# Kernel optimization log

Hardware: AMD Instinct MI355X
Metric: run time of the kernel (lower is better)

The kernel has to match this reference:

```python
import jax, jax.numpy as jnp
import numpy as np

PATCH = 16
IMG = 457
PAD = 7
HEADS = 8
NEG = -1e30        # finite stand-in for -inf (underflows to exactly 0 after softmax)


def layernorm(x, w, b):
    m = jnp.mean(x, axis=-1, keepdims=True)
    v = jnp.var(x, axis=-1, keepdims=True)
    return (x - m) / jnp.sqrt(v + 1e-5) * w + b


def shifted_patch_tokenize(x, w, b):
    # x: [B, C, H, W] (H, W multiples of PATCH)
    p = PATCH
    B, C, H, W = x.shape
    h = p // 2
    # torch order: (dx, dy) pairs, rolled as shifts=(dy, dx) over dims (2, 3)
    shifts = [(0, 0), (-h, -h), (h, -h), (-h, h), (h, h)]
    xs = jnp.concatenate(
        [jnp.roll(x, shift=(dy, dx), axis=(2, 3)) for dx, dy in shifts], axis=1
    )  # [B, 5C, H, W]
    Hp, Wp = H // p, W // p
    t = xs.reshape(B, 5 * C, Hp, p, Wp, p)
    t = t.transpose(0, 2, 4, 1, 3, 5).reshape(B, Hp * Wp, 5 * C * p * p)
    return t @ w.T + b  # [B, N, dim]


def locality_self_attention(x, scale, wqkv, wout, bout):
    # x: [B, N, C]; scale: [heads, 1, 1]
    B, N, C = x.shape
    dh = C // HEADS
    qkv = x @ wqkv.T  # [B, N, 3C]
    q, k, v = jnp.split(qkv, 3, axis=-1)
    q, k, v = [t.reshape(B, N, HEADS, dh).transpose(0, 2, 1, 3) for t in (q, k, v)]
    dots = jnp.einsum('bhid,bhjd->bhij', q, k) * scale[None]  # [B, H, N, N]
    idx = jnp.arange(N)
    mask = idx[None, :] >= idx[:, None]  # strict upper triangle + diagonal masked
    dots = jnp.where(mask, NEG, dots)
    attn = jax.nn.softmax(dots, axis=-1)
    # row 0 is fully masked (torch produces NaN here; we define it as 0 attention)
    attn = jnp.where(idx[:, None] == 0, 0.0, attn)
    out = jnp.einsum('bhij,bhjd->bhid', attn, v)
    out = out.transpose(0, 2, 1, 3).reshape(B, N, C)
    return out @ wout.T + bout


def reference(x, pos_emb, spt_w, spt_b, ln1_w, ln1_b, scale, wqkv, wout, bout,
              ln2_w, ln2_b, ff1_w, ff1_b, ff2_w, ff2_b, pix_w, pix_b):
    xp = jnp.pad(x, ((0, 0), (0, 0), (0, PAD), (0, PAD)))
    B, C, H, W = xp.shape
    p = PATCH
    Hp, Wp = H // p, W // p
    t = shifted_patch_tokenize(xp, spt_w, spt_b) + pos_emb  # [B, N, dim]
    depth = ln1_w.shape[0]
    for d in range(depth):
        t = locality_self_attention(layernorm(t, ln1_w[d], ln1_b[d]),
                                    scale[d], wqkv[d], wout[d], bout[d]) + t
        h = layernorm(t, ln2_w[d], ln2_b[d])
        h = jax.nn.gelu(h @ ff1_w[d].T + ff1_b[d], approximate=False)
        t = h @ ff2_w[d].T + ff2_b[d] + t
    pix = t @ pix_w.T + pix_b  # [B, N, C*p*p]
    out = pix.reshape(B, Hp, Wp, C, p, p).transpose(0, 3, 1, 4, 2, 5).reshape(B, C, H, W)
    return out[:, :, :IMG, :IMG]


def setup_inputs():
    key = jax.random.key(0)
    ks = jax.random.split(key, 10)
    B, Cin, dim, depth = 8, 1, 256, 3
    Np = 29 * 29  # padded 464/16 = 29 patches per side

    def rn(k, shape, sc=0.02):
        return jax.random.normal(k, shape, dtype=jnp.float32) * sc

    return {
        'x': jax.random.normal(ks[0], (B, Cin, IMG, IMG), dtype=jnp.float32),
        'pos_emb': rn(ks[1], (1, Np, dim), 1.0),
        'spt_w': rn(ks[2], (dim, Cin * 5 * PATCH * PATCH)),
        'spt_b': jnp.zeros((dim,), jnp.float32),
        'ln1_w': jnp.ones((depth, dim), jnp.float32),
        'ln1_b': jnp.zeros((depth, dim), jnp.float32),
        'scale': jnp.ones((depth, HEADS, 1, 1), jnp.float32),
        'wqkv': rn(ks[3], (depth, 3 * dim, dim)),
        'wout': rn(ks[4], (depth, dim, dim)),
        'bout': jnp.zeros((depth, dim), jnp.float32),
        'ln2_w': jnp.ones((depth, dim), jnp.float32),
        'ln2_b': jnp.zeros((depth, dim), jnp.float32),
        'ff1_w': rn(ks[5], (depth, 4 * dim, dim)),
        'ff1_b': jnp.zeros((depth, 4 * dim), jnp.float32),
        'ff2_w': rn(ks[6], (depth, dim, 4 * dim)),
        'ff2_b': jnp.zeros((depth, dim), jnp.float32),
        'pix_w': rn(ks[7], (Cin * PATCH * PATCH, dim)),
        'pix_b': jnp.zeros((Cin * PATCH * PATCH,), jnp.float32),
    }
```

## Files before the change

kernel.cpp:

```cpp
#include <hip/hip_runtime.h>
#include <hip/hip_bf16.h>
#include <math.h>

typedef __hip_bfloat16 bf16;
typedef short bf16x8 __attribute__((ext_vector_type(8)));
typedef float floatx4 __attribute__((ext_vector_type(4)));

#define NTOK 841
#define BATCH 8
#define DIM 256
#define HEADS 8
#define DH 32
#define IMG 457
#define HPAD 464
#define ROWS (BATCH * NTOK)
#define LDA 40

#define W_SPT   0
#define W_QKV   327680
#define W_OUT   917504
#define W_FF1   1114112
#define W_FF2   1900544
#define W_PIX   2686976
#define W_TOTAL 2752512

__device__ __forceinline__ float fast_gelu(float v) {
    float x = v * 0.70710678118654752f;
    float ax = fabsf(x);
    float t = __builtin_amdgcn_rcpf(1.0f + 0.3275911f * ax);
    float p = t * (0.254829592f +
              t * (-0.284496736f +
              t * (1.421413741f +
              t * (-1.453152027f +
              t * 1.061405429f))));
    float e = __expf(-x * x);
    float erfa = 1.0f - p * e;
    float erfx = copysignf(erfa, x);
    return 0.5f * v * (1.0f + erfx);
}

__global__ __launch_bounds__(256) void wconv_kernel(
    const float* __restrict__ s_spt, const float* __restrict__ s_qkv,
    const float* __restrict__ s_out, const float* __restrict__ s_ff1,
    const float* __restrict__ s_ff2, const float* __restrict__ s_pix,
    bf16* __restrict__ dst) {
    int idx = (blockIdx.x * 256 + threadIdx.x) * 4;
    const float* src; int off;
    if      (idx < W_QKV) { src = s_spt; off = W_SPT; }
    else if (idx < W_OUT) { src = s_qkv; off = W_QKV; }
    else if (idx < W_FF1) { src = s_out; off = W_OUT; }
    else if (idx < W_FF2) { src = s_ff1; off = W_FF1; }
    else if (idx < W_PIX) { src = s_ff2; off = W_FF2; }
    else                  { src = s_pix; off = W_PIX; }
    float4 v = *(const float4*)(src + (idx - off));
    union { ushort4 u; bf16 h[4]; } pk;
    pk.h[0] = __float2bfloat16(v.x);
    pk.h[1] = __float2bfloat16(v.y);
    pk.h[2] = __float2bfloat16(v.z);
    pk.h[3] = __float2bfloat16(v.w);
    *(ushort4*)(dst + idx) = pk.u;
}

__global__ __launch_bounds__(256) void tokenize_kernel(const float* __restrict__ x,
                                                       bf16* __restrict__ tok) {
    int idx = blockIdx.x * 256 + threadIdx.x;
    int gm = idx / 320;
    int k4 = (idx - gm * 320) * 4;
    int b = gm / NTOK;
    int n = gm - b * NTOK;
    int hp = n / 29, wp = n - (n / 29) * 29;
    int c = k4 >> 8;
    int py = (k4 >> 4) & 15;
    int px0 = k4 & 15;
    const int dxs[5] = {0, -8, 8, -8, 8};
    const int dys[5] = {0, -8, -8, 8, 8};
    int r = hp * 16 + py - dys[c];
    r += (r < 0) ? HPAD : 0; r -= (r >= HPAD) ? HPAD : 0;
    bool rok = (r < IMG);
    union { ushort4 u; bf16 h[4]; } pk;
#pragma unroll
    for (int i = 0; i < 4; i++) {
        int s = wp * 16 + px0 + i - dxs[c];
        s += (s < 0) ? HPAD : 0; s -= (s >= HPAD) ? HPAD : 0;
        float v = 0.0f;
        if (rok && s < IMG) v = x[((size_t)b * IMG + r) * IMG + s];
        pk.h[i] = __float2bfloat16(v);
    }
    *(ushort4*)(tok + (size_t)gm * 1280 + k4) = pk.u;
}

template <int BM, int BN>
__global__ __launch_bounds__(256) void gemm_db_kernel(
    const bf16* __restrict__ A, const bf16* __restrict__ W,
    const float* __restrict__ bias, const float* __restrict__ resid,
    const float* __restrict__ posemb, float* __restrict__ Cf,
    bf16* __restrict__ Cb, int M, int N, int K, int act) {
    constexpr int WM = BM / 2, WN = BN / 2;
    constexpr int TI = WM / 16, TJ = WN / 16;
    constexpr int ACHUNKS = BM * 4;
    constexpr int BCHUNKS = BN * 4;
    static_assert(ACHUNKS <= 256 && BCHUNKS <= 256, "one chunk per thread");
    __shared__ bf16 As[2][BM * LDA];
    __shared__ bf16 Bs[2][BN * LDA];
    const int tid = threadIdx.x;
    const int m0 = blockIdx.y * BM, n0 = blockIdx.x * BN;
    const int w = tid >> 6, lane = tid & 63;
    const int wm = (w >> 1) * WM, wn = (w & 1) * WN;
    const int li = lane & 15, quad = lane >> 4;

    floatx4 acc[TI][TJ] = {};
    float4 a0, b0, a1, b1;

    const int arow = tid >> 2, ako = (tid & 3) << 3;
    const bool a_on = tid < ACHUNKS;
    const bool b_on = tid < BCHUNKS;

    auto load_a = [&](float4& ar, int k0) {
        if (a_on) {
            int gm = m0 + arow;
            ar = make_float4(0.f, 0.f, 0.f, 0.f);
            if (gm < M) ar = *(const float4*)(A + (size_t)gm * K + k0 + ako);
        }
    };
    auto load_b = [&](float4& br, int k0) {
        if (b_on) br = *(const float4*)(W + (size_t)(n0 + arow) * K + k0 + ako);
    };
    auto store_ab = [&](int buf, const float4& ar, const float4& br) {
        if (a_on) *(float4*)&As[buf][arow * LDA + ako] = ar;
        if (b_on) *(float4*)&Bs[buf][arow * LDA + ako] = br;
    };
    auto compute = [&](int buf) {
        bf16x8 af[TI], bfr[TJ];
#pragma unroll
        for (int t = 0; t < TI; t++)
            af[t] = *(const bf16x8*)&As[buf][(wm + t * 16 + li) * LDA + quad * 8];
#pragma unroll
        for (int t = 0; t < TJ; t++)
            bfr[t] = *(const bf16x8*)&Bs[buf][(wn + t * 16 + li) * LDA + quad * 8];
#pragma unroll
        for (int ti = 0; ti < TI; ti++)
#pragma unroll
            for (int tj = 0; tj < TJ; tj++)
                acc[ti][tj] = __builtin_amdgcn_mfma_f32_16x16x32_bf16(
                    af[ti], bfr[tj], acc[ti][tj], 0, 0, 0);
    };

    const int ktiles = K >> 5;
    load_a(a0, 0); load_b(b0, 0);
    store_ab(0, a0, b0);
    if (ktiles > 1) { load_a(a0, 32); load_b(b0, 32); }
    if (ktiles > 2) { load_a(a1, 64); load_b(b1, 64); }
    __syncthreads();

    for (int kt = 0; kt < ktiles; kt += 2) {
        compute(0);
        if (kt + 1 < ktiles) store_ab(1, a0, b0);
        if (kt + 3 < ktiles) { load_a(a0, (kt + 3) << 5); load_b(b0, (kt + 3) << 5); }
        __syncthreads();
        compute(1);
        if (kt + 2 < ktiles) store_ab(0, a1, b1);
        if (kt + 4 < ktiles) { load_a(a1, (kt + 4) << 5); load_b(b1, (kt + 4) << 5); }
        __syncthreads();
    }

#pragma unroll
    for (int ti = 0; ti < TI; ti++) {
#pragma unroll
        for (int r = 0; r < 4; r++) {
            int gm = m0 + wm + ti * 16 + quad * 4 + r;
            if (gm >= M) continue;
#pragma unroll
            for (int tj = 0; tj < TJ; tj++) {
                int gn = n0 + wn + tj * 16 + li;
                float v = acc[ti][tj][r];
                if (bias) v += bias[gn];
                if (act == 1) v = fast_gelu(v);
                if (posemb) v += posemb[(size_t)(gm % NTOK) * N + gn];
                if (resid) v += resid[(size_t)gm * N + gn];
                if (Cf) Cf[(size_t)gm * N + gn] = v;
                if (Cb) Cb[(size_t)gm * N + gn] = __float2bfloat16(v);
            }
        }
    }
}

__global__ __launch_bounds__(256) void ln_kernel(const float* __restrict__ in,
                                                 const float* __restrict__ w,
                                                 const float* __restrict__ b,
                                                 bf16* __restrict__ out) {
    const int lane = threadIdx.x & 63;
    const int wv = threadIdx.x >> 6;
    const size_t row = (size_t)blockIdx.x * 4 + wv;
    const int c = lane * 4;
    float4 x = *(const float4*)&in[row * DIM + c];
    float s = x.x + x.y + x.z + x.w;
    float s2 = x.x * x.x + x.y * x.y + x.z * x.z + x.w * x.w;
#pragma unroll
    for (int off = 1; off < 64; off <<= 1) {
        s += __shfl_xor(s, off);
        s2 += __shfl_xor(s2, off);
    }
    float mean = s * (1.0f / DIM);
    float var = s2 * (1.0f / DIM) - mean * mean;
    float rstd = rsqrtf(var + 1e-5f);
    float4 w4 = *(const float4*)&w[c];
    float4 b4 = *(const float4*)&b[c];
    union { ushort4 u; bf16 h[4]; } pk;
    pk.h[0] = __float2bfloat16((x.x - mean) * rstd * w4.x + b4.x);
    pk.h[1] = __float2bfloat16((x.y - mean) * rstd * w4.y + b4.y);
    pk.h[2] = __float2bfloat16((x.z - mean) * rstd * w4.z + b4.z);
    pk.h[3] = __float2bfloat16((x.w - mean) * rstd * w4.w + b4.w);
    *(ushort4*)&out[row * DIM + c] = pk.u;
}

#define LQ 40
#define LP 72
__global__ __launch_bounds__(256) void attn_mfma_kernel(
    const bf16* __restrict__ qkv, const float* __restrict__ scale,
    bf16* __restrict__ out) {
    __shared__ bf16 Qs[64 * LQ];
    __shared__ bf16 Ks[2][64 * LQ];
    __shared__ bf16 Vt[2][32 * LP];
    __shared__ bf16 Ps[64 * LP];

    const int tid = threadIdx.x;
    const int bh = blockIdx.x;
    const int b = bh >> 3, h = bh & 7;
    const int it = (int)gridDim.y - 1 - (int)blockIdx.y;
    const int i0 = it * 64;
    const float sc = scale[h];
    const float sc2 = sc * 1.44269504f;
    const float mshift = -8.0f * 1.44269504f;
    const bf16* base = qkv + (size_t)b * NTOK * 768 + h * DH;

    const int w = tid >> 6, lane = tid & 63;
    const int li = lane & 15, quad = lane >> 4;
    const int srow = tid >> 2, sd0 = (tid & 3) * 8;
    const int vcol = (srow + ((tid & 3) << 4)) & 63;

    {
        int gi = i0 + srow;
        bf16x8 v = {};
        if (gi < NTOK) v = *(const bf16x8*)(base + (size_t)gi * 768 + sd0);
        *(bf16x8*)&Qs[srow * LQ + sd0] = v;
    }
    bf16x8 kreg = {}, vreg = {};
    {
        int gj = srow;
        if (gj < NTOK) {
            kreg = *(const bf16x8*)(base + (size_t)gj * 768 + 256 + sd0);
            vreg = *(const bf16x8*)(base + (size_t)gj * 768 + 512 + sd0);
        }
    }
    __syncthreads();
    const bf16x8 aq = *(const bf16x8*)&Qs[(w * 16 + li) * LQ + quad * 8];

    const bf16x8 ones8 = {(short)0x3F80, (short)0x3F80, (short)0x3F80, (short)0x3F80,
                          (short)0x3F80, (short)0x3F80, (short)0x3F80, (short)0x3F80};

    floatx4 o[2] = {};
    floatx4 o2 = {};
    const bool interior_ok = (i0 + 63 < NTOK);

    for (int jt = 0; jt <= it; jt++) {
        const int j0 = jt * 64;
        const int cur = jt & 1;
        *(bf16x8*)&Ks[cur][srow * LQ + sd0] = kreg;
#pragma unroll
        for (int u = 0; u < 8; u++) Vt[cur][(sd0 + u) * LP + vcol] = ((bf16*)&vreg)[u];
        if (jt < it) {
            int gj = j0 + 64 + srow;
            kreg = bf16x8{};
            vreg = bf16x8{};
            if (gj < NTOK) {
                kreg = *(const bf16x8*)(base + (size_t)gj * 768 + 256 + sd0);
                vreg = *(const bf16x8*)(base + (size_t)gj * 768 + 512 + sd0);
            }
        }
        __syncthreads();

        floatx4 sacc[4];
#pragma unroll
        for (int tj = 0; tj < 4; tj++) {
            bf16x8 bk = *(const bf16x8*)&Ks[cur][(tj * 16 + li) * LQ + quad * 8];
            floatx4 z = {};
            sacc[tj] = __builtin_amdgcn_mfma_f32_16x16x32_bf16(aq, bk, z, 0, 0, 0);
        }

        if (jt < it && interior_ok) {
#pragma unroll
            for (int r = 0; r < 4; r++) {
#pragma unroll
                for (int tj = 0; tj < 4; tj++) {
                    float p = exp2f(fmaf(sacc[tj][r], sc2, mshift));
                    Ps[(w * 16 + quad * 4 + r) * LP + tj * 16 + li] = __float2bfloat16(p);
                }
            }
        } else {
#pragma unroll
            for (int r = 0; r < 4; r++) {
                const int gi = i0 + w * 16 + quad * 4 + r;
#pragma unroll
                for (int tj = 0; tj < 4; tj++) {
                    bool ok = (j0 + tj * 16 + li < gi) && (gi < NTOK);
                    float arg = ok ? fmaf(sacc[tj][r], sc2, mshift) : -1e30f;
                    float p = exp2f(arg);
                    Ps[(w * 16 + quad * 4 + r) * LP + tj * 16 + li] = __float2bfloat16(p);
                }
            }
        }

#pragma unroll
        for (int kk = 0; kk < 64; kk += 32) {
            bf16x8 ap = *(const bf16x8*)&Ps[(w * 16 + li) * LP + kk + quad * 8];
#pragma unroll
            for (int td = 0; td < 2; td++) {
                const int kr = (2 * td + (li >> 3)) & 3;
                const int vc0 = (kk + quad * 8 + (kr << 4)) & 63;
                bf16x8 bv = *(const bf16x8*)&Vt[cur][(td * 16 + li) * LP + vc0];
                o[td] = __builtin_amdgcn_mfma_f32_16x16x32_bf16(ap, bv, o[td], 0, 0, 0);
            }
            o2 = __builtin_amdgcn_mfma_f32_16x16x32_bf16(ap, ones8, o2, 0, 0, 0);
        }
    }

#pragma unroll
    for (int r = 0; r < 4; r++) {
        int gi = i0 + w * 16 + quad * 4 + r;
        if (gi >= NTOK) continue;
        float l = o2[r];
        float iv = (gi > 0 && l > 0.0f) ? 1.0f / l : 0.0f;
        bf16* op = out + ((size_t)b * NTOK + gi) * DIM + h * DH;
        op[li]      = __float2bfloat16(o[0][r] * iv);
        op[16 + li] = __float2bfloat16(o[1][r] * iv);
    }
}

__global__ __launch_bounds__(256) void scatter_kernel(const float* __restrict__ pix,
                                                      float* __restrict__ out) {
    const size_t total = (size_t)BATCH * IMG * IMG;
    size_t idx = (size_t)blockIdx.x * 256 + threadIdx.x;
    if (idx >= total) return;
    int b = (int)(idx / ((size_t)IMG * IMG));
    int rem = (int)(idx % ((size_t)IMG * IMG));
    int r = rem / IMG, col = rem % IMG;
    int hp = r >> 4, py = r & 15;
    int wp = col >> 4, px = col & 15;
    out[idx] = pix[((size_t)b * NTOK + hp * 29 + wp) * DIM + py * 16 + px];
}

extern "C" void kernel_launch(void* const* d_in, const int* in_sizes, int n_in,
                              void* d_out, int out_size, void* d_ws, size_t ws_size,
                              hipStream_t stream) {
    const float* x     = (const float*)d_in[0];
    const float* pos   = (const float*)d_in[1];
    const float* sptw  = (const float*)d_in[2];
    const float* sptb  = (const float*)d_in[3];
    const float* ln1w  = (const float*)d_in[4];
    const float* ln1b  = (const float*)d_in[5];
    const float* scale = (const float*)d_in[6];
    const float* wqkv  = (const float*)d_in[7];
    const float* wout  = (const float*)d_in[8];
    const float* bout  = (const float*)d_in[9];
    const float* ln2w  = (const float*)d_in[10];
    const float* ln2b  = (const float*)d_in[11];
    const float* ff1w  = (const float*)d_in[12];
    const float* ff1b  = (const float*)d_in[13];
    const float* ff2w  = (const float*)d_in[14];
    const float* ff2b  = (const float*)d_in[15];
    const float* pixw  = (const float*)d_in[16];
    const float* pixb  = (const float*)d_in[17];
    float* out = (float*)d_out;

    const size_t NT = (size_t)ROWS * DIM;
    char* ws = (char*)d_ws;
    float* t    = (float*)ws;                         ws += NT * 4;
    bf16*  tn_b = (bf16*)ws;                          ws += NT * 2;
    bf16*  t_b  = (bf16*)ws;                          ws += NT * 2;
    bf16*  ao_b = (bf16*)ws;                          ws += NT * 2;
    bf16*  wbf  = (bf16*)ws;                          ws += (size_t)W_TOTAL * 2;
    char*  big  = ws;
    bf16*  tok   = (bf16*)big;
    bf16*  qkv_b = (bf16*)big;
    bf16*  ffh   = (bf16*)big;
    float* pixo  = (float*)big;

    wconv_kernel<<<W_TOTAL / 4 / 256, 256, 0, stream>>>(sptw, wqkv, wout, ff1w,
                                                        ff2w, pixw, wbf);
    tokenize_kernel<<<(ROWS * 320) / 256, 256, 0, stream>>>(x, tok);
    gemm_db_kernel<32, 64><<<dim3(4, 211), 256, 0, stream>>>(
        tok, wbf + W_SPT, sptb, nullptr, pos, t, nullptr, ROWS, DIM, 1280, 0);

    for (int d = 0; d < 3; d++) {
        ln_kernel<<<ROWS / 4, 256, 0, stream>>>(t, ln1w + d * DIM, ln1b + d * DIM, tn_b);
        gemm_db_kernel<64, 64><<<dim3(12, 106), 256, 0, stream>>>(
            tn_b, wbf + W_QKV + (size_t)d * 768 * DIM, nullptr, nullptr, nullptr,
            nullptr, qkv_b, ROWS, 768, DIM, 0);
        {
            dim3 grid(BATCH * HEADS, (NTOK + 63) / 64);
            attn_mfma_kernel<<<grid, 256, 0, stream>>>(qkv_b, scale + d * HEADS, ao_b);
        }
        gemm_db_kernel<32, 64><<<dim3(4, 211), 256, 0, stream>>>(
            ao_b, wbf + W_OUT + (size_t)d * DIM * DIM, bout + d * DIM, t, nullptr,
            t, nullptr, ROWS, DIM, DIM, 0);
        ln_kernel<<<ROWS / 4, 256, 0, stream>>>(t, ln2w + d * DIM, ln2b + d * DIM, tn_b);
        gemm_db_kernel<64, 64><<<dim3(16, 106), 256, 0, stream>>>(
            tn_b, wbf + W_FF1 + (size_t)d * 1024 * DIM, ff1b + d * 1024, nullptr,
            nullptr, nullptr, ffh, ROWS, 1024, DIM, 1);
        gemm_db_kernel<32, 64><<<dim3(4, 211), 256, 0, stream>>>(
            ffh, wbf + W_FF2 + (size_t)d * DIM * 1024, ff2b + d * DIM, t, nullptr,
            t, (d == 2) ? t_b : nullptr, ROWS, DIM, 1024, 0);
    }

    gemm_db_kernel<32, 64><<<dim3(4, 211), 256, 0, stream>>>(
        t_b, wbf + W_PIX, pixb, nullptr, nullptr, pixo, nullptr, ROWS, DIM, DIM, 0);
    {
        size_t total = (size_t)BATCH * IMG * IMG;
        scatter_kernel<<<dim3((unsigned)((total + 255) / 256)), 256, 0, stream>>>(pixo, out);
    }
}
```

Measured before the change: 335.8 us.

## Split-K with atomic residual accumulation for out-proj and FF2 GEMMs

Result: slower. 559.2 us (+66.5%).

```diff
diff --git a/kernel.cpp b/kernel.cpp
--- a/kernel.cpp
+++ b/kernel.cpp
@@ -94,7 +94,7 @@
     const bf16* __restrict__ A, const bf16* __restrict__ W,
     const float* __restrict__ bias, const float* __restrict__ resid,
     const float* __restrict__ posemb, float* __restrict__ Cf,
-    bf16* __restrict__ Cb, int M, int N, int K, int act) {
+    bf16* __restrict__ Cb, int M, int N, int K, int act, int kspl, int aF32) {
     constexpr int WM = BM / 2, WN = BN / 2;
     constexpr int TI = WM / 16, TJ = WN / 16;
     constexpr int ACHUNKS = BM * 4;
@@ -119,7 +119,25 @@
         if (a_on) {
             int gm = m0 + arow;
             ar = make_float4(0.f, 0.f, 0.f, 0.f);
-            if (gm < M) ar = *(const float4*)(A + (size_t)gm * K + k0 + ako);
+            if (gm < M) {
+                if (aF32) {
+                    const float* Af = (const float*)A;
+                    float4 u0 = *(const float4*)(Af + (size_t)gm * K + k0 + ako);
+                    float4 u1 = *(const float4*)(Af + (size_t)gm * K + k0 + ako + 4);
+                    union { float4 f; ushort s[8]; } pk;
+                    pk.s[0] = __bfloat16_as_ushort(__float2bfloat16(u0.x));
+                    pk.s[1] = __bfloat16_as_ushort(__float2bfloat16(u0.y));
+                    pk.s[2] = __bfloat16_as_ushort(__float2bfloat16(u0.z));
+                    pk.s[3] = __bfloat16_as_ushort(__float2bfloat16(u0.w));
+                    pk.s[4] = __bfloat16_as_ushort(__float2bfloat16(u1.x));
+                    pk.s[5] = __bfloat16_as_ushort(__float2bfloat16(u1.y));
+                    pk.s[6] = __bfloat16_as_ushort(__float2bfloat16(u1.z));
+                    pk.s[7] = __bfloat16_as_ushort(__float2bfloat16(u1.w));
+                    ar = pk.f;
+                } else {
+                    ar = *(const float4*)(A + (size_t)gm * K + k0 + ako);
+                }
+            }
         }
     };
     auto load_b = [&](float4& br, int k0) {
@@ -145,22 +163,44 @@
                     af[ti], bfr[tj], acc[ti][tj], 0, 0, 0);
     };
 
-    const int ktiles = K >> 5;
-    load_a(a0, 0); load_b(b0, 0);
+    const int ktotal = K >> 5;
+    const int kts = ktotal / kspl;
+    const int ktb = blockIdx.z * kts;
+    load_a(a0, ktb << 5); load_b(b0, ktb << 5);
     store_ab(0, a0, b0);
-    if (ktiles > 1) { load_a(a0, 32); load_b(b0, 32); }
-    if (ktiles > 2) { load_a(a1, 64); load_b(b1, 64); }
+    if (kts > 1) { load_a(a0, (ktb + 1) << 5); load_b(b0, (ktb + 1) << 5); }
+    if (kts > 2) { load_a(a1, (ktb + 2) << 5); load_b(b1, (ktb + 2) << 5); }
     __syncthreads();
 
-    for (int kt = 0; kt < ktiles; kt += 2) {
+    for (int kt = 0; kt < kts; kt += 2) {
         compute(0);
-        if (kt + 1 < ktiles) store_ab(1, a0, b0);
-        if (kt + 3 < ktiles) { load_a(a0, (kt + 3) << 5); load_b(b0, (kt + 3) << 5); }
+        if (kt + 1 < kts) store_ab(1, a0, b0);
+        if (kt + 3 < kts) { load_a(a0, (ktb + kt + 3) << 5); load_b(b0, (ktb + kt + 3) << 5); }
         __syncthreads();
         compute(1);
-        if (kt + 2 < ktiles) store_ab(0, a1, b1);
-        if (kt + 4 < ktiles) { load_a(a1, (kt + 4) << 5); load_b(b1, (kt + 4) << 5); }
+        if (kt + 2 < kts) store_ab(0, a1, b1);
+        if (kt + 4 < kts) { load_a(a1, (ktb + kt + 4) << 5); load_b(b1, (ktb + kt + 4) << 5); }
         __syncthreads();
+    }
+
+    if (kspl > 1) {
+        const bool addb = (blockIdx.z == 0) && (bias != nullptr);
+#pragma unroll
+        for (int ti = 0; ti < TI; ti++) {
+#pragma unroll
+            for (int r = 0; r < 4; r++) {
+                int gm = m0 + wm + ti * 16 + quad * 4 + r;
+                if (gm >= M) continue;
+#pragma unroll
+                for (int tj = 0; tj < TJ; tj++) {
+                    int gn = n0 + wn + tj * 16 + li;
+                    float v = acc[ti][tj][r];
+                    if (addb) v += bias[gn];
+                    atomicAdd(&Cf[(size_t)gm * N + gn], v);
+                }
+            }
+        }
+        return;
     }
 
 #pragma unroll
@@ -376,7 +416,6 @@
     char* ws = (char*)d_ws;
     float* t    = (float*)ws;                         ws += NT * 4;
     bf16*  tn_b = (bf16*)ws;                          ws += NT * 2;
-    bf16*  t_b  = (bf16*)ws;                          ws += NT * 2;
     bf16*  ao_b = (bf16*)ws;                          ws += NT * 2;
     bf16*  wbf  = (bf16*)ws;                          ws += (size_t)W_TOTAL * 2;
     char*  big  = ws;
@@ -389,31 +428,32 @@
                                                         ff2w, pixw, wbf);
     tokenize_kernel<<<(ROWS * 320) / 256, 256, 0, stream>>>(x, tok);
     gemm_db_kernel<32, 64><<<dim3(4, 211), 256, 0, stream>>>(
-        tok, wbf + W_SPT, sptb, nullptr, pos, t, nullptr, ROWS, DIM, 1280, 0);
+        tok, wbf + W_SPT, sptb, nullptr, pos, t, nullptr, ROWS, DIM, 1280, 0, 1, 0);
 
     for (int d = 0; d < 3; d++) {
         ln_kernel<<<ROWS / 4, 256, 0, stream>>>(t, ln1w + d * DIM, ln1b + d * DIM, tn_b);
         gemm_db_kernel<64, 64><<<dim3(12, 106), 256, 0, stream>>>(
             tn_b, wbf + W_QKV + (size_t)d * 768 * DIM, nullptr, nullptr, nullptr,
-            nullptr, qkv_b, ROWS, 768, DIM, 0);
+            nullptr, qkv_b, ROWS, 768, DIM, 0, 1, 0);
         {
             dim3 grid(BATCH * HEADS, (NTOK + 63) / 64);
             attn_mfma_kernel<<<grid, 256, 0, stream>>>(qkv_b, scale + d * HEADS, ao_b);
         }
-        gemm_db_kernel<32, 64><<<dim3(4, 211), 256, 0, stream>>>(
-            ao_b, wbf + W_OUT + (size_t)d * DIM * DIM, bout + d * DIM, t, nullptr,
-            t, nullptr, ROWS, DIM, DIM, 0);
+        gemm_db_kernel<32, 64><<<dim3(4, 211, 2), 256, 0, stream>>>(
+            ao_b, wbf + W_OUT + (size_t)d * DIM * DIM, bout + d * DIM, nullptr,
+            nullptr, t, nullptr, ROWS, DIM, DIM, 0, 2, 0);
         ln_kernel<<<ROWS / 4, 256, 0, stream>>>(t, ln2w + d * DIM, ln2b + d * DIM, tn_b);
         gemm_db_kernel<64, 64><<<dim3(16, 106), 256, 0, stream>>>(
             tn_b, wbf + W_FF1 + (size_t)d * 1024 * DIM, ff1b + d * 1024, nullptr,
-            nullptr, nullptr, ffh, ROWS, 1024, DIM, 1);
-        gemm_db_kernel<32, 64><<<dim3(4, 211), 256, 0, stream>>>(
-            ffh, wbf + W_FF2 + (size_t)d * DIM * 1024, ff2b + d * DIM, t, nullptr,
-            t, (d == 2) ? t_b : nullptr, ROWS, DIM, 1024, 0);
+            nullptr, nullptr, ffh, ROWS, 1024, DIM, 1, 1, 0);
+        gemm_db_kernel<32, 64><<<dim3(4, 211, 4), 256, 0, stream>>>(
+            ffh, wbf + W_FF2 + (size_t)d * DIM * 1024, ff2b + d * DIM, nullptr,
+            nullptr, t, nullptr, ROWS, DIM, 1024, 0, 4, 0);
     }
 
     gemm_db_kernel<32, 64><<<dim3(4, 211), 256, 0, stream>>>(
-        t_b, wbf + W_PIX, pixb, nullptr, nullptr, pixo, nullptr, ROWS, DIM, DIM, 0);
+        (const bf16*)t, wbf + W_PIX, pixb, nullptr, nullptr, pixo, nullptr,
+        ROWS, DIM, DIM, 0, 1, 1);
     {
         size_t total = (size_t)BATCH * IMG * IMG;
         scatter_kernel<<<dim3((unsigned)((total + 255) / 256)), 256, 0, stream>>>(pixo, out);
```
